# Kernel optimization log

Measured on AMD Instinct MI355X. Metric: run time of the kernel, lower is better.

## Reference

```python
import jax, jax.numpy as jnp
import numpy as np

B = 16384      # games
BS = 19        # board size
N2 = BS * BS   # 361
G = 8          # groups per board
S = 4          # stones per group
R = B * G      # total groups
K = R * S      # total stones
M = N2         # hash history length (H*W*history_factor)
I32MIN = np.iinfo(np.int32).min
I32MAX = np.iinfo(np.int32).max
NEG = jnp.float32(-1e9)


def setup_inputs() -> dict:
    key = jax.random.key(0)
    ks = jax.random.split(key, 10)
    logits = jax.random.normal(ks[0], (B, BS, BS), dtype=jnp.float32)
    legal_mask = jax.random.uniform(ks[1], (B, BS, BS)) < 0.7
    current_player = jax.random.randint(ks[2], (B,), 0, 2, dtype=jnp.int32)
    current_hash = jax.random.randint(ks[3], (B,), 0, I32MAX, dtype=jnp.int32)
    hash_history = jax.random.randint(ks[4], (B, M), 0, I32MAX, dtype=jnp.int32)
    move_count = jax.random.randint(ks[5], (B,), 0, M, dtype=jnp.int32)
    ZposT = jax.random.randint(ks[6], (3, N2), 0, I32MAX, dtype=jnp.int32)
    stone_global_index = jax.random.randint(ks[7], (K,), 0, N2, dtype=jnp.int32)
    stone_global_pointer = jnp.arange(R + 1, dtype=jnp.int32) * S          # CSR: stones per group
    group_global_pointer_per_board = jnp.arange(B + 1, dtype=jnp.int32) * G  # CSR: groups per board
    cap_idx = jax.random.randint(ks[8], (B, N2, 4), 0, G, dtype=jnp.int32)
    cap_on = jax.random.uniform(ks[9], (B, N2, 4)) < 0.05
    captured_group_local_index = jnp.where(cap_on, cap_idx, jnp.int32(-1))
    return {
        "logits": logits,
        "legal_mask": legal_mask,
        "current_player": current_player,
        "current_hash": current_hash,
        "hash_history": hash_history,
        "move_count": move_count,
        "ZposT": ZposT,
        "stone_global_index": stone_global_index,
        "stone_global_pointer": stone_global_pointer,
        "group_global_pointer_per_board": group_global_pointer_per_board,
        "captured_group_local_index": captured_group_local_index,
    }


def reference(logits, legal_mask, current_player, current_hash, hash_history,
              move_count, ZposT, stone_global_index, stone_global_pointer,
              group_global_pointer_per_board, captured_group_local_index):
    Bn, H, W = legal_mask.shape
    Rn = stone_global_pointer.shape[0] - 1
    Kn = stone_global_index.shape[0]
    z_empty, z_black, z_white = ZposT[0], ZposT[1], ZposT[2]

    # Placement delta: empty -> current player's stone, for every candidate point. (B, N2)
    placement_delta = z_empty[None, :] ^ jnp.where(
        (current_player == 0)[:, None], z_black[None, :], z_white[None, :])

    # Map each group -> board, each stone -> group (CSR expansion).
    groups_per_board = group_global_pointer_per_board[1:] - group_global_pointer_per_board[:-1]
    group_board = jnp.repeat(jnp.arange(Bn, dtype=jnp.int32), groups_per_board,
                             total_repeat_length=Rn)
    stones_per_group = stone_global_pointer[1:] - stone_global_pointer[:-1]
    group_for_stone = jnp.repeat(jnp.arange(Rn, dtype=jnp.int32), stones_per_group,
                                 total_repeat_length=Kn)
    stone_board = group_board[group_for_stone]

    # Per-stone removal delta: opponent stone -> empty.
    opp_for_stone = (1 - current_player)[stone_board]           # (K,)
    si = stone_global_index.astype(jnp.int32)
    z_opp = ZposT[1 + opp_for_stone, si]
    per_stone_delta = z_opp ^ z_empty[si]                        # (K,) int32

    # Segmented XOR reduction over each group's stones via XOR prefix scan.
    prefix = jax.lax.associative_scan(jnp.bitwise_xor, per_stone_delta)
    start = stone_global_pointer[:-1]
    end = stone_global_pointer[1:]
    end_val = prefix[jnp.clip(end - 1, 0)]
    start_val = jnp.where(start > 0, prefix[jnp.clip(start - 1, 0)], jnp.int32(0))
    group_xor = end_val ^ start_val                              # (R,) per-group removal delta

    # Gather capture deltas for up to 4 captured neighbor groups per candidate move.
    offs = group_global_pointer_per_board[:-1][:, None, None]    # (B,1,1)
    flat_ids = jnp.clip(captured_group_local_index, 0) + offs    # (B,N2,4)
    cap_vals = jnp.where(captured_group_local_index >= 0, group_xor[flat_ids], jnp.int32(0))
    capture_delta = cap_vals[..., 0] ^ cap_vals[..., 1] ^ cap_vals[..., 2] ^ cap_vals[..., 3]

    candidate = current_hash[:, None] ^ placement_delta ^ capture_delta  # (B, N2)

    # Super-ko repeat detection against hash history (mask, sort, searchsorted).
    Mh = hash_history.shape[1]
    valid = jnp.arange(Mh, dtype=jnp.int32)[None, :] < jnp.minimum(move_count, Mh)[:, None]
    masked_hist = jnp.where(valid, hash_history, jnp.int32(I32MIN))
    sorted_hist = jnp.sort(masked_hist, axis=1)
    idx = jnp.clip(
        jax.vmap(lambda h, c: jnp.searchsorted(h, c, side='right'))(sorted_hist, candidate) - 1,
        0)
    found = jnp.take_along_axis(sorted_hist, idx, axis=1)
    repeat = (found == candidate).reshape(Bn, H, W)

    final_mask = legal_mask & ~repeat
    return jnp.where(final_mask, logits, NEG)
```

## Files before the change

kernel.cpp:

```cpp
#include <hip/hip_runtime.h>
#include <stdint.h>

#define N2 361
#define TBLW 1024
#define TBL_MASK 1023u
#define EMPTY_SLOT 0x80000000u
#define NEGV -998244352.0f

__global__ __launch_bounds__(256, 4) void go_repeat_mask_kernel(
    const float* __restrict__ logits,
    const void*  __restrict__ legal_raw,
    const int*   __restrict__ current_player,
    const int*   __restrict__ current_hash,
    const int*   __restrict__ hash_history,
    const int*   __restrict__ move_count,
    const int*   __restrict__ ZposT,
    const int*   __restrict__ stone_global_index,
    const int*   __restrict__ stone_global_pointer,
    const int*   __restrict__ group_global_pointer,
    const int4*  __restrict__ captured4,
    float*       __restrict__ out,
    int packed_bits)
{
    __shared__ unsigned s_table[4 * TBLW];

    const int tid  = threadIdx.x;
    const int wid  = tid >> 6;
    const int lane = tid & 63;
    const int b    = __builtin_amdgcn_readfirstlane(blockIdx.x * 4 + wid);
    unsigned* tbl  = s_table + wid * TBLW;
    const size_t bbase = (size_t)b * N2;

    const int      cp  = current_player[b];
    const unsigned ch  = (unsigned)current_hash[b];
    int            cnt = move_count[b];

    const int*  hist  = hash_history + bbase;
    const int4* hist4 = (const int4*)hist;
    const int4  ha    = hist4[lane];
    const int4  hb    = (lane < 26) ? hist4[64 + lane] : int4{0,0,0,0};
    const int   hc    = (lane == 26) ? hist[360] : 0;

    const unsigned* lwd = (const unsigned*)legal_raw;
    const unsigned dv0 = lwd[lane];
    const unsigned dv1 = (lane < 27) ? lwd[64 + lane] : 0u;

    int sp0 = 0, sp1 = 0;
    const int g0 = group_global_pointer[b];
    const int g1 = group_global_pointer[b + 1];
    if (lane < 32) {
        const int r = g0 + (lane >> 2);
        if (r < g1) { sp0 = stone_global_pointer[r]; sp1 = stone_global_pointer[r + 1]; }
    }

    int4  cap[6];
    float lg[6];
    unsigned zA[6], zB[6];
    const int prow = (1 + cp) * N2;
    #pragma unroll
    for (int s = 0; s < 6; ++s) {
        const int n = lane + 64 * s;
        const int nc = (n < N2) ? n : (N2 - 1);
        const size_t q = bbase + nc;
        cap[s] = captured4[q];
        lg[s]  = logits[q];
        zA[s]  = (unsigned)ZposT[nc];
        zB[s]  = (unsigned)ZposT[prow + nc];
    }

    auto classify = [](unsigned v) -> unsigned {
        unsigned f = 0;
        #pragma unroll
        for (int j = 0; j < 4; ++j) {
            const unsigned bv = (v >> (8 * j)) & 0xFFu;
            if (bv > 1u) f |= 1u;
            if (j != 0 && bv != 0u) f |= 2u;
        }
        const unsigned x = v & 0xFFFFu, y = v >> 16;
        if ((x && x != 0x3F80u) || (y && y != 0x3F80u)) f |= 4u;
        if (x == 0x3F80u) f |= 8u;
        return f;
    };
    unsigned fcl = classify(dv0);
    if (lane < 27) fcl |= classify(dv1);
    unsigned fa = 0;
    fa |= __ballot(fcl & 1u) ? 1u : 0u;
    fa |= __ballot(fcl & 2u) ? 2u : 0u;
    fa |= __ballot(fcl & 4u) ? 4u : 0u;
    fa |= __ballot(fcl & 8u) ? 8u : 0u;

    int fmt;
    if (packed_bits) fmt = 4;
    else if (!(fa & 1u)) fmt = 0;
    else if (!(fa & 4u)) fmt = (fa & 8u) ? 2 : 0;
    else fmt = 1;

    unsigned leg[6];
    #pragma unroll
    for (int s = 0; s < 6; ++s) leg[s] = 0u;
    {
        #pragma unroll
        for (int s = 0; s < 6; ++s) {
            const int n = lane + 64 * s;
            const size_t q = bbase + ((n < N2) ? n : (N2 - 1));
            if (fmt == 0)      leg[s] = ((const unsigned*)legal_raw)[q];
            else if (fmt == 1) leg[s] = ((const uint8_t*)legal_raw)[q];
            else if (fmt == 2) leg[s] = ((const uint16_t*)legal_raw)[q];
            else               leg[s] = (((const uint8_t*)legal_raw)[q >> 3] >> (q & 7)) & 1u;
        }
    }

    unsigned gx = 0u;
    if (lane < 32) {
        const int j = lane & 3;
        const int opprow = (2 - cp) * N2;
        for (int k = sp0 + j; k < sp1; k += 4) {
            const int si = stone_global_index[k];
            gx ^= (unsigned)ZposT[opprow + si] ^ (unsigned)ZposT[si];
        }
        gx ^= __shfl_xor(gx, 1);
        gx ^= __shfl_xor(gx, 2);
    }

    {
        uint4* t4 = (uint4*)tbl;
        const uint4 e4 = {EMPTY_SLOT, EMPTY_SLOT, EMPTY_SLOT, EMPTY_SLOT};
        #pragma unroll
        for (int i = 0; i < 4; ++i) t4[lane + 64 * i] = e4;
    }

    cnt = cnt < 0 ? 0 : (cnt > N2 ? N2 : cnt);

    auto ins = [&](unsigned v) {
        unsigned slot = v & TBL_MASK;
        while (true) {
            const unsigned old = atomicCAS(&tbl[slot], EMPTY_SLOT, v);
            if (old == EMPTY_SLOT || old == v) break;
            slot = (slot + 1) & TBL_MASK;
        }
    };
    {
        const int i0 = 4 * lane;
        if (i0 + 0 < cnt) ins((unsigned)ha.x);
        if (i0 + 1 < cnt) ins((unsigned)ha.y);
        if (i0 + 2 < cnt) ins((unsigned)ha.z);
        if (i0 + 3 < cnt) ins((unsigned)ha.w);
        if (lane < 26) {
            const int i1 = 256 + 4 * lane;
            if (i1 + 0 < cnt) ins((unsigned)hb.x);
            if (i1 + 1 < cnt) ins((unsigned)hb.y);
            if (i1 + 2 < cnt) ins((unsigned)hb.z);
            if (i1 + 3 < cnt) ins((unsigned)hb.w);
        }
        if (lane == 26 && 360 < cnt) ins((unsigned)hc);
    }
    asm volatile("s_waitcnt lgkmcnt(0)" ::: "memory");

    auto probe = [&](unsigned cand) -> bool {
        unsigned slot = cand & TBL_MASK;
        while (true) {
            const unsigned v = tbl[slot];
            if (v == cand) return true;
            if (v == EMPTY_SLOT) return false;
            slot = (slot + 1) & TBL_MASK;
        }
    };
    #pragma unroll
    for (int s = 0; s < 6; ++s) {
        const int n = lane + 64 * s;
        if (n < N2) {
            unsigned capd = 0u;
            const int4 c = cap[s];
            if (c.x >= 0) capd ^= (unsigned)__shfl((int)gx, (c.x & 7) * 4);
            if (c.y >= 0) capd ^= (unsigned)__shfl((int)gx, (c.y & 7) * 4);
            if (c.z >= 0) capd ^= (unsigned)__shfl((int)gx, (c.z & 7) * 4);
            if (c.w >= 0) capd ^= (unsigned)__shfl((int)gx, (c.w & 7) * 4);
            const unsigned cand = ch ^ zA[s] ^ zB[s] ^ capd;
            const float v = (leg[s] && !probe(cand)) ? lg[s] : NEGV;
            __builtin_nontemporal_store(v, &out[bbase + n]);
        }
    }
}

extern "C" void kernel_launch(void* const* d_in, const int* in_sizes, int n_in,
                              void* d_out, int out_size, void* d_ws, size_t ws_size,
                              hipStream_t stream) {
    const float* logits  = (const float*)d_in[0];
    const void*  legal   = (const void*)d_in[1];
    const int*   cur_pl  = (const int*)d_in[2];
    const int*   cur_h   = (const int*)d_in[3];
    const int*   hist    = (const int*)d_in[4];
    const int*   mcount  = (const int*)d_in[5];
    const int*   zpos    = (const int*)d_in[6];
    const int*   sgi     = (const int*)d_in[7];
    const int*   sgp     = (const int*)d_in[8];
    const int*   ggp     = (const int*)d_in[9];
    const int4*  cap4    = (const int4*)d_in[10];
    float*       out     = (float*)d_out;

    const int B = in_sizes[2];
    const int packed = (in_sizes[1] != in_sizes[0]);

    go_repeat_mask_kernel<<<B / 4, 256, 0, stream>>>(
        logits, legal, cur_pl, cur_h, hist, mcount, zpos,
        sgi, sgp, ggp, cap4, out, packed);
}
```

Before: 228.1 us.

## Replace shared-memory hash table with bitmap filter plus wave-wide exact match

Swaps the per-board open-addressing hash table (CAS inserts, linear-probe lookups) for a 32K-bit shared-memory bitmap filled with atomicOr. Candidates that hit a set bit are checked exactly by broadcasting each one across the wave and comparing against the 9 history values each lane holds in registers. This removes CAS retry loops and divergent probe chains. In exchange it adds a serial ballot/shuffle loop per filter hit, and that cost grows with the false-positive rate. It also precombines the two Zobrist loads into one XOR.

```diff
diff --git a/kernel.cpp b/kernel.cpp
--- a/kernel.cpp
+++ b/kernel.cpp
@@ -2,9 +2,8 @@
 #include <stdint.h>
 
 #define N2 361
-#define TBLW 1024
-#define TBL_MASK 1023u
-#define EMPTY_SLOT 0x80000000u
+#define BMW 1024u
+#define EMPTY 0x80000000u
 #define NEGV -998244352.0f
 
 __global__ __launch_bounds__(256, 4) void go_repeat_mask_kernel(
@@ -22,18 +21,19 @@
     float*       __restrict__ out,
     int packed_bits)
 {
-    __shared__ unsigned s_table[4 * TBLW];
+    __shared__ unsigned s_bm[4 * BMW];
 
     const int tid  = threadIdx.x;
     const int wid  = tid >> 6;
     const int lane = tid & 63;
     const int b    = __builtin_amdgcn_readfirstlane(blockIdx.x * 4 + wid);
-    unsigned* tbl  = s_table + wid * TBLW;
+    unsigned* bm   = s_bm + wid * BMW;
     const size_t bbase = (size_t)b * N2;
 
     const int      cp  = current_player[b];
     const unsigned ch  = (unsigned)current_hash[b];
     int            cnt = move_count[b];
+    cnt = cnt < 0 ? 0 : (cnt > N2 ? N2 : cnt);
 
     const int*  hist  = hash_history + bbase;
     const int4* hist4 = (const int4*)hist;
@@ -55,17 +55,16 @@
 
     int4  cap[6];
     float lg[6];
-    unsigned zA[6], zB[6];
+    unsigned zz[6];
     const int prow = (1 + cp) * N2;
     #pragma unroll
     for (int s = 0; s < 6; ++s) {
-        const int n = lane + 64 * s;
+        const int n  = lane + 64 * s;
         const int nc = (n < N2) ? n : (N2 - 1);
         const size_t q = bbase + nc;
         cap[s] = captured4[q];
         lg[s]  = logits[q];
-        zA[s]  = (unsigned)ZposT[nc];
-        zB[s]  = (unsigned)ZposT[prow + nc];
+        zz[s]  = (unsigned)ZposT[nc] ^ (unsigned)ZposT[prow + nc];
     }
 
     auto classify = [](unsigned v) -> unsigned {
@@ -97,17 +96,20 @@
 
     unsigned leg[6];
     #pragma unroll
-    for (int s = 0; s < 6; ++s) leg[s] = 0u;
+    for (int s = 0; s < 6; ++s) {
+        const int n = lane + 64 * s;
+        const size_t q = bbase + ((n < N2) ? n : (N2 - 1));
+        if (fmt == 0)      leg[s] = ((const unsigned*)legal_raw)[q];
+        else if (fmt == 1) leg[s] = ((const uint8_t*)legal_raw)[q];
+        else if (fmt == 2) leg[s] = ((const uint16_t*)legal_raw)[q];
+        else               leg[s] = (((const uint8_t*)legal_raw)[q >> 3] >> (q & 7)) & 1u;
+    }
+
     {
+        uint4* t4 = (uint4*)bm;
+        const uint4 z4 = {0u, 0u, 0u, 0u};
         #pragma unroll
-        for (int s = 0; s < 6; ++s) {
-            const int n = lane + 64 * s;
-            const size_t q = bbase + ((n < N2) ? n : (N2 - 1));
-            if (fmt == 0)      leg[s] = ((const unsigned*)legal_raw)[q];
-            else if (fmt == 1) leg[s] = ((const uint8_t*)legal_raw)[q];
-            else if (fmt == 2) leg[s] = ((const uint16_t*)legal_raw)[q];
-            else               leg[s] = (((const uint8_t*)legal_raw)[q >> 3] >> (q & 7)) & 1u;
-        }
+        for (int i = 0; i < 4; ++i) t4[lane + 64 * i] = z4;
     }
 
     unsigned gx = 0u;
@@ -122,61 +124,63 @@
         gx ^= __shfl_xor(gx, 2);
     }
 
-    {
-        uint4* t4 = (uint4*)tbl;
-        const uint4 e4 = {EMPTY_SLOT, EMPTY_SLOT, EMPTY_SLOT, EMPTY_SLOT};
-        #pragma unroll
-        for (int i = 0; i < 4; ++i) t4[lane + 64 * i] = e4;
-    }
-
-    cnt = cnt < 0 ? 0 : (cnt > N2 ? N2 : cnt);
-
-    auto ins = [&](unsigned v) {
-        unsigned slot = v & TBL_MASK;
-        while (true) {
-            const unsigned old = atomicCAS(&tbl[slot], EMPTY_SLOT, v);
-            if (old == EMPTY_SLOT || old == v) break;
-            slot = (slot + 1) & TBL_MASK;
-        }
+    const int i0 = 4 * lane;
+    const int i1 = 256 + 4 * lane;
+    unsigned e0 = (i0 + 0 < cnt) ? (unsigned)ha.x : EMPTY;
+    unsigned e1 = (i0 + 1 < cnt) ? (unsigned)ha.y : EMPTY;
+    unsigned e2 = (i0 + 2 < cnt) ? (unsigned)ha.z : EMPTY;
+    unsigned e3 = (i0 + 3 < cnt) ? (unsigned)ha.w : EMPTY;
+    unsigned e4 = (lane < 26 && i1 + 0 < cnt) ? (unsigned)hb.x : EMPTY;
+    unsigned e5 = (lane < 26 && i1 + 1 < cnt) ? (unsigned)hb.y : EMPTY;
+    unsigned e6 = (lane < 26 && i1 + 2 < cnt) ? (unsigned)hb.z : EMPTY;
+    unsigned e7 = (lane < 26 && i1 + 3 < cnt) ? (unsigned)hb.w : EMPTY;
+    unsigned e8 = (lane == 26 && 360 < cnt)   ? (unsigned)hc   : EMPTY;
+
+    asm volatile("s_waitcnt lgkmcnt(0)" ::: "memory");
+    __builtin_amdgcn_sched_barrier(0);
+
+    auto setbit = [&](unsigned v) {
+        if (!(v & EMPTY)) atomicOr(&bm[(v >> 5) & (BMW - 1u)], 1u << (v & 31u));
     };
-    {
-        const int i0 = 4 * lane;
-        if (i0 + 0 < cnt) ins((unsigned)ha.x);
-        if (i0 + 1 < cnt) ins((unsigned)ha.y);
-        if (i0 + 2 < cnt) ins((unsigned)ha.z);
-        if (i0 + 3 < cnt) ins((unsigned)ha.w);
-        if (lane < 26) {
-            const int i1 = 256 + 4 * lane;
-            if (i1 + 0 < cnt) ins((unsigned)hb.x);
-            if (i1 + 1 < cnt) ins((unsigned)hb.y);
-            if (i1 + 2 < cnt) ins((unsigned)hb.z);
-            if (i1 + 3 < cnt) ins((unsigned)hb.w);
-        }
-        if (lane == 26 && 360 < cnt) ins((unsigned)hc);
-    }
+    setbit(e0); setbit(e1); setbit(e2); setbit(e3);
+    setbit(e4); setbit(e5); setbit(e6); setbit(e7); setbit(e8);
+
     asm volatile("s_waitcnt lgkmcnt(0)" ::: "memory");
-
-    auto probe = [&](unsigned cand) -> bool {
-        unsigned slot = cand & TBL_MASK;
-        while (true) {
-            const unsigned v = tbl[slot];
-            if (v == cand) return true;
-            if (v == EMPTY_SLOT) return false;
-            slot = (slot + 1) & TBL_MASK;
-        }
+    __builtin_amdgcn_sched_barrier(0);
+
+    unsigned cand[6], bw[6];
+    #pragma unroll
+    for (int s = 0; s < 6; ++s) {
+        unsigned capd = 0u;
+        const int4 c = cap[s];
+        if (c.x >= 0) capd ^= (unsigned)__shfl((int)gx, (c.x & 7) * 4);
+        if (c.y >= 0) capd ^= (unsigned)__shfl((int)gx, (c.y & 7) * 4);
+        if (c.z >= 0) capd ^= (unsigned)__shfl((int)gx, (c.z & 7) * 4);
+        if (c.w >= 0) capd ^= (unsigned)__shfl((int)gx, (c.w & 7) * 4);
+        cand[s] = ch ^ zz[s] ^ capd;
+        bw[s] = bm[(cand[s] >> 5) & (BMW - 1u)];
+    }
+
+    auto match9 = [&](unsigned c) -> bool {
+        return (e0 == c) | (e1 == c) | (e2 == c) | (e3 == c) |
+               (e4 == c) | (e5 == c) | (e6 == c) | (e7 == c) | (e8 == c);
     };
+
     #pragma unroll
     for (int s = 0; s < 6; ++s) {
         const int n = lane + 64 * s;
-        if (n < N2) {
-            unsigned capd = 0u;
-            const int4 c = cap[s];
-            if (c.x >= 0) capd ^= (unsigned)__shfl((int)gx, (c.x & 7) * 4);
-            if (c.y >= 0) capd ^= (unsigned)__shfl((int)gx, (c.y & 7) * 4);
-            if (c.z >= 0) capd ^= (unsigned)__shfl((int)gx, (c.z & 7) * 4);
-            if (c.w >= 0) capd ^= (unsigned)__shfl((int)gx, (c.w & 7) * 4);
-            const unsigned cand = ch ^ zA[s] ^ zB[s] ^ capd;
-            const float v = (leg[s] && !probe(cand)) ? lg[s] : NEGV;
+        const bool inr = n < N2;
+        bool rep = false;
+        unsigned long long mask = __ballot(inr && ((bw[s] >> (cand[s] & 31u)) & 1u));
+        while (mask) {
+            const int l = __ffsll((unsigned long long)mask) - 1;
+            const unsigned c = (unsigned)__shfl((int)cand[s], l);
+            const unsigned long long fm = __ballot(match9(c));
+            if (lane == l) rep = (fm != 0ull);
+            mask &= mask - 1;
+        }
+        if (inr) {
+            const float v = (leg[s] && !rep) ? lg[s] : NEGV;
             __builtin_nontemporal_store(v, &out[bbase + n]);
         }
     }
```

After: 221.7 us. 2.8% less time.
